# Performance work log

Measured on AMD Instinct MI355X. Metric: run time of the kernel, lower is better.

## Reference

```python
import jax, jax.numpy as jnp
import numpy as np

HIDDEN = 32
ODE_H = 0.1      # rk4 fixed step size (torchdiffeq options step_size=0.1)
ODE_STEPS = 10   # integrate t in [0, 1]


def gcn_conv(x, W, b, edge_index, n):
    """PyG GCNConv: symmetric norm with self-loops; x' = D^-1/2 (A+I) D^-1/2 (x W) + b."""
    h = x @ W                                  # [n, out]
    src, dst = edge_index[0], edge_index[1]
    deg = jnp.ones((n,), h.dtype).at[dst].add(1.0)   # +1 for self-loop
    dinv = jax.lax.rsqrt(deg)
    coef = (dinv[src] * dinv[dst])[:, None]
    agg = jnp.zeros_like(h).at[dst].add(h[src] * coef)
    agg = agg + h * (dinv * dinv)[:, None]     # self-loop term
    return agg + b


def ode_rk4(x0, edge_index, Wg, bg, wt, n):
    """RK4 integration of psi(t,x)=relu(GCN(x)) * sigmoid(t * wt) from t=0 to 1."""
    def f(t, x):
        gate = jax.nn.sigmoid(t * wt)          # [hidden], Linear(1,h,no bias).sigmoid()
        return jax.nn.relu(gcn_conv(x, Wg, bg, edge_index, n)) * gate

    h = ODE_H
    def step(x, t):
        k1 = f(t, x)
        k2 = f(t + h * 0.5, x + (h * 0.5) * k1)
        k3 = f(t + h * 0.5, x + (h * 0.5) * k2)
        k4 = f(t + h, x + h * k3)
        return x + (h / 6.0) * (k1 + 2.0 * k2 + 2.0 * k3 + k4), None

    ts = jnp.arange(ODE_STEPS, dtype=x0.dtype) * h
    xf, _ = jax.lax.scan(step, x0, ts)
    return xf


def setup_inputs() -> dict:
    key = jax.random.key(0)
    ks = jax.random.split(key, 16)
    N, IN, H = 100000, 128, HIDDEN
    E, DE = 1600000, 800000

    inp = {
        "H_t": jax.random.normal(ks[0], (N, IN), jnp.float32),
        "A_pos_t": jax.random.randint(ks[1], (2, E), 0, N),
        "A_neg_t": jax.random.randint(ks[2], (2, E), 0, N),
        "dA_pos": jax.random.randint(ks[3], (2, DE), 0, N),
        "dA_neg": jax.random.randint(ks[4], (2, DE), 0, N),
        # init GCN
        "W_init": jax.random.normal(ks[5], (IN, H), jnp.float32) / np.sqrt(IN),
        "b_init": jnp.zeros((H,), jnp.float32),
        # pos ODE func
        "W_pos": jax.random.normal(ks[6], (H, H), jnp.float32) / np.sqrt(H),
        "b_pos": jnp.zeros((H,), jnp.float32),
        "wt_pos": jax.random.normal(ks[7], (H,), jnp.float32),
        # neg ODE func
        "W_neg": jax.random.normal(ks[8], (H, H), jnp.float32) / np.sqrt(H),
        "b_neg": jnp.zeros((H,), jnp.float32),
        "wt_neg": jax.random.normal(ks[9], (H,), jnp.float32),
        # combine + layernorm
        "W_comb": jax.random.normal(ks[10], (2 * H, H), jnp.float32) / np.sqrt(2 * H),
        "b_comb": jnp.zeros((H,), jnp.float32),
        "ln_g": jnp.ones((H,), jnp.float32),
        "ln_b": jnp.zeros((H,), jnp.float32),
    }
    return inp


def reference(H_t, A_pos_t, A_neg_t, dA_pos, dA_neg,
              W_init, b_init, W_pos, b_pos, wt_pos,
              W_neg, b_neg, wt_neg, W_comb, b_comb, ln_g, ln_b):
    n = H_t.shape[0]
    edges_all = jnp.concatenate([A_pos_t, A_neg_t], axis=1)
    H = jax.nn.relu(gcn_conv(H_t, W_init, b_init, edges_all, n))   # [n, hidden]
    Z_pos = ode_rk4(H, dA_pos, W_pos, b_pos, wt_pos, n)
    Z_neg = ode_rk4(H, dA_neg, W_neg, b_neg, wt_neg, n)
    Z = jnp.concatenate([Z_pos, Z_neg], axis=-1) @ W_comb + b_comb # [n, hidden]
    mu = jnp.mean(Z, axis=-1, keepdims=True)
    var = jnp.var(Z, axis=-1, keepdims=True)
    return (Z - mu) * jax.lax.rsqrt(var + 1e-5) * ln_g + ln_b
```

## Files before the change

### kernel.cpp

```cpp
#include <hip/hip_runtime.h>
#include <math.h>


#define TPB 256
#define SCAN_T 1024
#define IDX_CAP 2048

typedef _Float16 h8 __attribute__((ext_vector_type(8)));
typedef float f8 __attribute__((ext_vector_type(8)));


struct Seg { const int* dst; int n; int* cnt; };
struct FSeg { const int* src; const int* dst; int n; const int* offs; int* cur; };

__global__ void count4(Seg s0, Seg s1, Seg s2, Seg s3) {
    int i = blockIdx.x * blockDim.x + threadIdx.x;
    Seg s; int e;
    if (i < s0.n) { s = s0; e = i; }
    else if (i < s0.n + s1.n) { s = s1; e = i - s0.n; }
    else if (i < s0.n + s1.n + s2.n) { s = s2; e = i - s0.n - s1.n; }
    else if (i < s0.n + s1.n + s2.n + s3.n) { s = s3; e = i - s0.n - s1.n - s2.n; }
    else return;
    atomicAdd(&s.cnt[s.dst[e]], 1);
}

__global__ void fill4(FSeg s0, FSeg s1, FSeg s2, FSeg s3, int* __restrict__ csr) {
    int i = blockIdx.x * blockDim.x + threadIdx.x;
    FSeg s; int e;
    if (i < s0.n) { s = s0; e = i; }
    else if (i < s0.n + s1.n) { s = s1; e = i - s0.n; }
    else if (i < s0.n + s1.n + s2.n) { s = s2; e = i - s0.n - s1.n; }
    else if (i < s0.n + s1.n + s2.n + s3.n) { s = s3; e = i - s0.n - s1.n - s2.n; }
    else return;
    int d = s.dst[e];
    int pos = s.offs[d] + atomicAdd(&s.cur[d], 1);
    csr[pos] = s.src[e];
}

__global__ void dinv_from_cnt(const int* __restrict__ cnt, float* __restrict__ dinv, int n) {
    int i = blockIdx.x * blockDim.x + threadIdx.x;
    if (i < n) dinv[i] = rsqrtf(1.0f + (float)cnt[i]);
}

__global__ void scan_block(const int* __restrict__ in, int n, int* __restrict__ out,
                           int* __restrict__ bsums) {
    __shared__ int sh[SCAN_T];
    int tx = threadIdx.x;
    int g = blockIdx.x * SCAN_T + tx;
    int v = (g < n) ? in[g] : 0;
    sh[tx] = v;
    __syncthreads();
    for (int off = 1; off < SCAN_T; off <<= 1) {
        int t = (tx >= off) ? sh[tx - off] : 0;
        __syncthreads();
        sh[tx] += t;
        __syncthreads();
    }
    if (g < n) out[g] = sh[tx] - v;
    if (tx == SCAN_T - 1) bsums[blockIdx.x] = sh[tx];
}

__global__ void scan_sums(int* __restrict__ bsums, int nb) {
    __shared__ int sh[SCAN_T];
    int tx = threadIdx.x;
    int v = (tx < nb) ? bsums[tx] : 0;
    sh[tx] = v;
    __syncthreads();
    for (int off = 1; off < SCAN_T; off <<= 1) {
        int t = (tx >= off) ? sh[tx - off] : 0;
        __syncthreads();
        sh[tx] += t;
        __syncthreads();
    }
    if (tx < nb) bsums[tx] = sh[tx] - v;
}

__global__ void scan_add(int* __restrict__ offs, const int* __restrict__ bsums, int n, int total) {
    int g = blockIdx.x * blockDim.x + threadIdx.x;
    if (g < n) offs[g] += bsums[g >> 10];
    if (g == 0) offs[n] = total;
}


__global__ void mm32_kernel(const float* __restrict__ x, const float* __restrict__ W,
                            const float* __restrict__ dinv, _Float16* __restrict__ hs, int N) {
    __shared__ float Ws[32][32];
    __shared__ float xs[8][32];
    int tid = threadIdx.x;
    for (int i = tid; i < 32 * 32; i += TPB) Ws[i >> 5][i & 31] = W[i];
    int base = blockIdx.x * 8;
    {
        int idx = base * 32 + tid;
        xs[tid >> 5][tid & 31] = (idx < N * 32) ? x[idx] : 0.0f;
    }
    __syncthreads();
    int row = tid >> 5, c = tid & 31;
    int gr = base + row;
    float acc = 0.0f;
#pragma unroll
    for (int k = 0; k < 32; ++k) acc += xs[row][k] * Ws[k][c];
    if (gr < N) hs[gr * 32 + c] = (_Float16)(acc * dinv[gr]);
}

__global__ void mm128_kernel(const float* __restrict__ x, const float* __restrict__ W,
                             const float* __restrict__ dinv, _Float16* __restrict__ hs, int N) {
    __shared__ float Ws[128][32];
    __shared__ float xs[8][128];
    int tid = threadIdx.x;
    for (int i = tid; i < 128 * 32; i += TPB) Ws[i >> 5][i & 31] = W[i];
    int base = blockIdx.x * 8;
    for (int i = tid; i < 8 * 128; i += TPB) {
        int idx = base * 128 + i;
        xs[i >> 7][i & 127] = (idx < N * 128) ? x[idx] : 0.0f;
    }
    __syncthreads();
    int row = tid >> 5, c = tid & 31;
    int gr = base + row;
    float acc = 0.0f;
#pragma unroll
    for (int k = 0; k < 128; ++k) acc += xs[row][k] * Ws[k][c];
    if (gr < N) hs[gr * 32 + c] = (_Float16)(acc * dinv[gr]);
}


struct Job {
    const int* offs; const int* csr;
    const _Float16* hs_in; _Float16* hs_out;
    const float* dinv; const float* dinv_next;
    const float* bias; const float* wt;
    float* ksum; float* x;
    const float* W;
};

__global__ __launch_bounds__(TPB) void agg_stage(Job jp, Job jn, int nbp, float t,
                                                 int stage, int do_mm, float* __restrict__ x2,
                                                 int N) {
    __shared__ float Ws[32][32];
    __shared__ float xts[64][36];
    __shared__ int sidx[IDX_CAP];
    __shared__ int soffs[65];

    bool isP = blockIdx.x < nbp;
    const Job& J = isP ? jp : jn;
    int bid = isP ? blockIdx.x : (blockIdx.x - nbp);
    int nbase = bid * 64;
    int tid = threadIdx.x;
    int lnode = tid >> 2, q = tid & 3;
    int node = nbase + lnode;
    bool valid = node < N;

    if (do_mm) {
        for (int i = tid; i < 32 * 32; i += TPB) Ws[i >> 5][i & 31] = J.W[i];
    }
    int nend = nbase + 64; if (nend > N) nend = N;
    int e_lo = J.offs[nbase];
    int e_hi = J.offs[nend];
    int cnt = e_hi - e_lo;
    int staged = cnt < IDX_CAP ? cnt : IDX_CAP;
    for (int i = tid; i < staged; i += TPB) sidx[i] = J.csr[e_lo + i];
    if (tid < 65) {
        int ix = nbase + tid; if (ix > N) ix = N;
        soffs[tid] = J.offs[ix];
    }
    __syncthreads();

    f8 xrow;
#pragma unroll
    for (int j = 0; j < 8; ++j) xrow[j] = 0.f;

    if (valid) {
        const h8* hsv = (const h8*)J.hs_in;
        int r0 = soffs[lnode] - e_lo;
        int r1 = soffs[lnode + 1] - e_lo;
        f8 acc = __builtin_convertvector(hsv[node * 4 + q], f8);
        int i = r0;
        int lim = r1 < staged ? r1 : staged;
        for (; i + 4 <= lim; i += 4) {
            h8 v0 = hsv[sidx[i] * 4 + q];
            h8 v1 = hsv[sidx[i + 1] * 4 + q];
            h8 v2 = hsv[sidx[i + 2] * 4 + q];
            h8 v3 = hsv[sidx[i + 3] * 4 + q];
            acc += (__builtin_convertvector(v0, f8) + __builtin_convertvector(v1, f8))
                 + (__builtin_convertvector(v2, f8) + __builtin_convertvector(v3, f8));
        }
        for (; i < lim; ++i)
            acc += __builtin_convertvector(hsv[sidx[i] * 4 + q], f8);
        for (; i < r1; ++i)
            acc += __builtin_convertvector(hsv[J.csr[e_lo + i] * 4 + q], f8);

        float dv = J.dinv[node];
        f8 bb = ((const f8*)J.bias)[q];
        f8 kv;
#pragma unroll
        for (int j = 0; j < 8; ++j) kv[j] = fmaxf(acc[j] * dv + bb[j], 0.f);
        if (J.wt) {
            f8 w = ((const f8*)J.wt)[q];
#pragma unroll
            for (int j = 0; j < 8; ++j) kv[j] *= 1.f / (1.f + expf(-t * w[j]));
        }
        int idx = node * 4 + q;
        f8* x8 = (f8*)J.x;
        f8* ks8 = (f8*)J.ksum;
        if (stage == 0) {
            x8[idx] = kv;
            ((f8*)x2)[idx] = kv;
            xrow = kv;
        } else if (stage == 4) {
            f8 ks = ks8[idx];
            f8 xv = x8[idx];
            const float cc = 0.1f / 6.0f;
#pragma unroll
            for (int j = 0; j < 8; ++j) xv[j] += cc * (ks[j] + kv[j]);
            x8[idx] = xv;
            xrow = xv;
        } else {
            float a = (stage == 3) ? 0.1f : 0.05f;
            f8 xv = x8[idx];
#pragma unroll
            for (int j = 0; j < 8; ++j) xrow[j] = xv[j] + a * kv[j];
            if (stage == 1) {
                ks8[idx] = kv;
            } else {
                f8 ks = ks8[idx];
#pragma unroll
                for (int j = 0; j < 8; ++j) ks[j] += 2.f * kv[j];
                ks8[idx] = ks;
            }
        }
    }

    if (do_mm) {
        if (valid) {
#pragma unroll
            for (int j = 0; j < 8; ++j) xts[lnode][q * 8 + j] = xrow[j];
        }
        __syncthreads();
        if (valid) {
            f8 accm;
#pragma unroll
            for (int j = 0; j < 8; ++j) accm[j] = 0.f;
#pragma unroll
            for (int k = 0; k < 32; ++k) {
                float xv = xts[lnode][k];
                f8 w = *(const f8*)&Ws[k][q * 8];
                accm += xv * w;
            }
            accm *= J.dinv_next[node];
            ((h8*)J.hs_out)[node * 4 + q] = __builtin_convertvector(accm, h8);
        }
    }
}


__global__ void combine_kernel(const float* __restrict__ zp, const float* __restrict__ zn,
                               const float* __restrict__ Wc, const float* __restrict__ bc,
                               const float* __restrict__ g, const float* __restrict__ be,
                               float* __restrict__ out, int N) {
    __shared__ float Ws[64][32];
    __shared__ float zs[8][64];
    int tid = threadIdx.x;
    for (int i = tid; i < 64 * 32; i += TPB) Ws[i >> 5][i & 31] = Wc[i];
    int base = blockIdx.x * 8;
    {
        int r = tid >> 5, c = tid & 31;
        int gr = base + r;
        zs[r][c] = (gr < N) ? zp[gr * 32 + c] : 0.0f;
        zs[r][32 + c] = (gr < N) ? zn[gr * 32 + c] : 0.0f;
    }
    __syncthreads();
    int row = tid >> 5, c = tid & 31;
    int gr = base + row;
    float acc = bc[c];
#pragma unroll
    for (int k = 0; k < 64; ++k) acc += zs[row][k] * Ws[k][c];
    float s = acc, sq = acc * acc;
#pragma unroll
    for (int off = 16; off; off >>= 1) {
        s += __shfl_xor(s, off, 32);
        sq += __shfl_xor(sq, off, 32);
    }
    float mu = s * (1.0f / 32.0f);
    float var = sq * (1.0f / 32.0f) - mu * mu;
    float y = (acc - mu) * rsqrtf(var + 1e-5f) * g[c] + be[c];
    if (gr < N) out[gr * 32 + c] = y;
}


extern "C" void kernel_launch(void* const* d_in, const int* in_sizes, int n_in,
                              void* d_out, int out_size, void* d_ws, size_t ws_size,
                              hipStream_t stream) {
    const float* H_t = (const float*)d_in[0];
    const int* Apos = (const int*)d_in[1];
    const int* Aneg = (const int*)d_in[2];
    const int* dApos = (const int*)d_in[3];
    const int* dAneg = (const int*)d_in[4];
    const float* W_init = (const float*)d_in[5];
    const float* b_init = (const float*)d_in[6];
    const float* W_pos = (const float*)d_in[7];
    const float* b_pos = (const float*)d_in[8];
    const float* wt_pos = (const float*)d_in[9];
    const float* W_neg = (const float*)d_in[10];
    const float* b_neg = (const float*)d_in[11];
    const float* wt_neg = (const float*)d_in[12];
    const float* W_comb = (const float*)d_in[13];
    const float* b_comb = (const float*)d_in[14];
    const float* ln_g = (const float*)d_in[15];
    const float* ln_b = (const float*)d_in[16];

    const int N = in_sizes[0] / 128;
    const int E1 = in_sizes[1] / 2;
    const int E2 = in_sizes[2] / 2;
    const int DE1 = in_sizes[3] / 2;
    const int DE2 = in_sizes[4] / 2;
    const int Etot = E1 + E2 + DE1 + DE2;

    const int* Apos_src = Apos, * Apos_dst = Apos + E1;
    const int* Aneg_src = Aneg, * Aneg_dst = Aneg + E2;
    const int* dApos_src = dApos, * dApos_dst = dApos + DE1;
    const int* dAneg_src = dAneg, * dAneg_dst = dAneg + DE2;

    const size_t n32 = (size_t)N * 32;
    const size_t szf = n32 * 4;
    const size_t szh = n32 * 2;
    auto al = [](size_t b) { return (b + 255) & ~(size_t)255; };

    size_t small_bytes = 3 * al((size_t)(3 * N) * 4)
                       + al((3 * (size_t)N + 1) * 4)
                       + al((size_t)Etot * 4)
                       + al(SCAN_T * 4);
    size_t need_merged = 4 * al(szf) + 4 * al(szh) + small_bytes;
    bool merged = ws_size >= need_merged + 4096;

    char* p = (char*)d_ws;
    auto alloc = [&](size_t bytes) -> void* {
        void* r = (void*)p;
        p += al(bytes);
        return r;
    };
    float* x_pos = (float*)alloc(szf);
    float* x_neg = (float*)alloc(szf);
    float* ksum_p = (float*)alloc(szf);
    float* ksum_n = merged ? (float*)alloc(szf) : ksum_p;
    _Float16* hs_pa = (_Float16*)alloc(szh);
    _Float16* hs_pb = (_Float16*)alloc(szh);
    _Float16* hs_na = merged ? (_Float16*)alloc(szh) : hs_pa;
    _Float16* hs_nb = merged ? (_Float16*)alloc(szh) : hs_pb;
    float* dinv3 = (float*)alloc((size_t)(3 * N) * 4);
    int* cnt3 = (int*)alloc((size_t)(3 * N) * 4);
    int* cur3 = (int*)alloc((size_t)(3 * N) * 4);
    int* offs3 = (int*)alloc((3 * (size_t)N + 1) * 4);
    int* csr3 = (int*)alloc((size_t)Etot * 4);
    int* bsums = (int*)alloc(SCAN_T * 4);

    size_t used = (size_t)(p - (char*)d_ws);
    if (used > ws_size) used = ws_size;

    hipMemsetAsync(d_ws, 0, used, stream);

    float* dinv_all = dinv3, * dinv_pos = dinv3 + N, * dinv_neg = dinv3 + 2 * N;
    int* cnt_all = cnt3, * cnt_pos = cnt3 + N, * cnt_neg = cnt3 + 2 * N;
    int* cur_all = cur3, * cur_pos = cur3 + N, * cur_neg = cur3 + 2 * N;
    const int* offs_all = offs3, * offs_pos = offs3 + N, * offs_neg = offs3 + 2 * N;

    dim3 blk(TPB);
    auto gblk = [](int n) { return dim3((n + TPB - 1) / TPB); };
    dim3 grid_rows((N + 7) / 8);
    const int nb64 = (N + 63) / 64;
    const int n3 = 3 * N;
    const int nbs = (n3 + SCAN_T - 1) / SCAN_T;

    {
        Seg s0 = { Apos_dst, E1, cnt_all };
        Seg s1 = { Aneg_dst, E2, cnt_all };
        Seg s2 = { dApos_dst, DE1, cnt_pos };
        Seg s3 = { dAneg_dst, DE2, cnt_neg };
        count4<<<gblk(Etot), blk, 0, stream>>>(s0, s1, s2, s3);
    }
    dinv_from_cnt<<<gblk(n3), blk, 0, stream>>>(cnt3, dinv3, n3);
    scan_block<<<nbs, SCAN_T, 0, stream>>>(cnt3, n3, offs3, bsums);
    scan_sums<<<1, SCAN_T, 0, stream>>>(bsums, nbs);
    scan_add<<<gblk(n3), blk, 0, stream>>>(offs3, bsums, n3, Etot);
    {
        FSeg f0 = { Apos_src, Apos_dst, E1, offs_all, cur_all };
        FSeg f1 = { Aneg_src, Aneg_dst, E2, offs_all, cur_all };
        FSeg f2 = { dApos_src, dApos_dst, DE1, offs_pos, cur_pos };
        FSeg f3 = { dAneg_src, dAneg_dst, DE2, offs_neg, cur_neg };
        fill4<<<gblk(Etot), blk, 0, stream>>>(f0, f1, f2, f3, csr3);
    }

    auto mkjob = [&](const int* offs, const _Float16* hs_in, _Float16* hs_out,
                     const float* dinv, const float* dinv_next, const float* bias,
                     const float* wt, float* ksum, float* x, const float* W) {
        Job j; j.offs = offs; j.csr = csr3; j.hs_in = hs_in; j.hs_out = hs_out;
        j.dinv = dinv; j.dinv_next = dinv_next; j.bias = bias; j.wt = wt;
        j.ksum = ksum; j.x = x; j.W = W; return j;
    };

    mm128_kernel<<<grid_rows, blk, 0, stream>>>(H_t, W_init, dinv_all, hs_pa, N);
    {
        Job j0 = mkjob(offs_all, hs_pa, hs_pb, dinv_all, dinv_pos, b_init,
                       nullptr, nullptr, x_pos, W_pos);
        agg_stage<<<nb64, blk, 0, stream>>>(j0, j0, nb64, 0.0f, 0, 1, x_neg, N);
    }

    if (merged) {
        mm32_kernel<<<grid_rows, blk, 0, stream>>>(x_neg, W_neg, dinv_neg, hs_nb, N);
        for (int s = 0; s < 10; ++s) {
            float t0 = 0.1f * (float)s;
            int last_mm = (s == 9) ? 0 : 1;
            Job p1 = mkjob(offs_pos, hs_pb, hs_pa, dinv_pos, dinv_pos, b_pos, wt_pos, ksum_p, x_pos, W_pos);
            Job n1 = mkjob(offs_neg, hs_nb, hs_na, dinv_neg, dinv_neg, b_neg, wt_neg, ksum_n, x_neg, W_neg);
            agg_stage<<<2 * nb64, blk, 0, stream>>>(p1, n1, nb64, t0, 1, 1, nullptr, N);
            Job p2 = p1; p2.hs_in = hs_pa; p2.hs_out = hs_pb;
            Job n2 = n1; n2.hs_in = hs_na; n2.hs_out = hs_nb;
            agg_stage<<<2 * nb64, blk, 0, stream>>>(p2, n2, nb64, t0 + 0.05f, 2, 1, nullptr, N);
            agg_stage<<<2 * nb64, blk, 0, stream>>>(p1, n1, nb64, t0 + 0.05f, 3, 1, nullptr, N);
            agg_stage<<<2 * nb64, blk, 0, stream>>>(p2, n2, nb64, t0 + 0.1f, 4, last_mm, nullptr, N);
        }
    } else {
        for (int ode = 0; ode < 2; ++ode) {
            float* x = ode ? x_neg : x_pos;
            const float* W = ode ? W_neg : W_pos;
            const float* b = ode ? b_neg : b_pos;
            const float* wt = ode ? wt_neg : wt_pos;
            const float* dinv = ode ? dinv_neg : dinv_pos;
            const int* offs = ode ? offs_neg : offs_pos;
            if (ode == 1) {
                mm32_kernel<<<grid_rows, blk, 0, stream>>>(x, W, dinv, hs_pb, N);
            }
            for (int s = 0; s < 10; ++s) {
                float t0 = 0.1f * (float)s;
                int last_mm = (s == 9) ? 0 : 1;
                Job j1 = mkjob(offs, hs_pb, hs_pa, dinv, dinv, b, wt, ksum_p, x, W);
                Job j2 = j1; j2.hs_in = hs_pa; j2.hs_out = hs_pb;
                agg_stage<<<nb64, blk, 0, stream>>>(j1, j1, nb64, t0, 1, 1, nullptr, N);
                agg_stage<<<nb64, blk, 0, stream>>>(j2, j2, nb64, t0 + 0.05f, 2, 1, nullptr, N);
                agg_stage<<<nb64, blk, 0, stream>>>(j1, j1, nb64, t0 + 0.05f, 3, 1, nullptr, N);
                agg_stage<<<nb64, blk, 0, stream>>>(j2, j2, nb64, t0 + 0.1f, 4, last_mm, nullptr, N);
            }
        }
    }

    combine_kernel<<<grid_rows, blk, 0, stream>>>(x_pos, x_neg, W_comb, b_comb, ln_g, ln_b,
                                                  (float*)d_out, N);
}
```

Measured before the change: 2.185 ms.

## Build CSR via two-pass radix bucketing and drop LDS index staging in aggregation

```diff
diff --git a/kernel.cpp b/kernel.cpp
--- a/kernel.cpp
+++ b/kernel.cpp
@@ -4,24 +4,25 @@
 
 #define TPB 256
 #define SCAN_T 1024
-#define IDX_CAP 2048
+#define RB 512
+#define PA_TILE 4096
 
 typedef _Float16 h8 __attribute__((ext_vector_type(8)));
 typedef float f8 __attribute__((ext_vector_type(8)));
 
 
-struct Seg { const int* dst; int n; int* cnt; };
+struct SegG { const int* src; const int* dst; int n; int goff; };
 struct FSeg { const int* src; const int* dst; int n; const int* offs; int* cur; };
 
-__global__ void count4(Seg s0, Seg s1, Seg s2, Seg s3) {
+__global__ void count4(SegG s0, SegG s1, SegG s2, SegG s3, int* __restrict__ cnt3) {
     int i = blockIdx.x * blockDim.x + threadIdx.x;
-    Seg s; int e;
+    SegG s; int e;
     if (i < s0.n) { s = s0; e = i; }
     else if (i < s0.n + s1.n) { s = s1; e = i - s0.n; }
     else if (i < s0.n + s1.n + s2.n) { s = s2; e = i - s0.n - s1.n; }
     else if (i < s0.n + s1.n + s2.n + s3.n) { s = s3; e = i - s0.n - s1.n - s2.n; }
     else return;
-    atomicAdd(&s.cnt[s.dst[e]], 1);
+    atomicAdd(&cnt3[s.goff + s.dst[e]], 1);
 }
 
 __global__ void fill4(FSeg s0, FSeg s1, FSeg s2, FSeg s3, int* __restrict__ csr) {
@@ -81,6 +82,83 @@
     if (g == 0) offs[n] = total;
 }
 
+__global__ void init_stage_cur(const int* __restrict__ offs3, int* __restrict__ stage_cur,
+                               int B, int n3) {
+    int b = blockIdx.x * blockDim.x + threadIdx.x;
+    if (b < B) {
+        int k = b << 10; if (k > n3) k = n3;
+        stage_cur[b] = offs3[k];
+    }
+}
+
+__global__ __launch_bounds__(TPB) void passA(SegG s0, SegG s1, SegG s2, SegG s3,
+                                             int* __restrict__ stage_cur,
+                                             int* __restrict__ staging, int Etot) {
+    __shared__ int lh[RB];
+    __shared__ int lbase[RB];
+    int tid = threadIdx.x;
+    int base = blockIdx.x * PA_TILE;
+    int t1 = s0.n, t2 = t1 + s1.n, t3 = t2 + s2.n;
+
+    for (int b = tid; b < RB; b += TPB) lh[b] = 0;
+    __syncthreads();
+
+    int gds[16], srcs[16];
+#pragma unroll
+    for (int k = 0; k < 16; ++k) {
+        int i = base + k * TPB + tid;
+        gds[k] = -1;
+        if (i < Etot) {
+            SegG s; int e;
+            if (i < t1) { s = s0; e = i; }
+            else if (i < t2) { s = s1; e = i - t1; }
+            else if (i < t3) { s = s2; e = i - t2; }
+            else { s = s3; e = i - t3; }
+            int gd = s.goff + s.dst[e];
+            gds[k] = gd;
+            srcs[k] = s.src[e];
+            atomicAdd(&lh[gd >> 10], 1);
+        }
+    }
+    __syncthreads();
+    for (int b = tid; b < RB; b += TPB) {
+        int c = lh[b];
+        lbase[b] = c ? atomicAdd(&stage_cur[b], c) : 0;
+    }
+    __syncthreads();
+    for (int b = tid; b < RB; b += TPB) lh[b] = 0;
+    __syncthreads();
+#pragma unroll
+    for (int k = 0; k < 16; ++k) {
+        int gd = gds[k];
+        if (gd >= 0) {
+            int b = gd >> 10;
+            int r = atomicAdd(&lh[b], 1);
+            staging[lbase[b] + r] = ((gd & 1023) << 17) | srcs[k];
+        }
+    }
+}
+
+__global__ __launch_bounds__(TPB) void passB(const int* __restrict__ staging,
+                                             const int* __restrict__ offs3,
+                                             int* __restrict__ cur3,
+                                             int* __restrict__ csr3, int n3) {
+    int b = blockIdx.x >> 3, sl = blockIdx.x & 7;
+    int k0 = b << 10;
+    int k1 = k0 + 1024; if (k1 > n3) k1 = n3;
+    if (k0 >= n3) return;
+    int lo = offs3[k0], hi = offs3[k1];
+    int len = hi - lo;
+    int c0 = lo + (int)((long long)len * sl / 8);
+    int c1 = lo + (int)((long long)len * (sl + 1) / 8);
+    for (int i = c0 + threadIdx.x; i < c1; i += TPB) {
+        int ent = staging[i];
+        int gd = k0 + (ent >> 17);
+        int pos = offs3[gd] + atomicAdd(&cur3[gd], 1);
+        csr3[pos] = ent & 0x1FFFF;
+    }
+}
+
 
 __global__ void mm32_kernel(const float* __restrict__ x, const float* __restrict__ W,
                             const float* __restrict__ dinv, _Float16* __restrict__ hs, int N) {
@@ -137,7 +215,6 @@
                                                  int N) {
     __shared__ float Ws[32][32];
     __shared__ float xts[64][36];
-    __shared__ int sidx[IDX_CAP];
     __shared__ int soffs[65];
 
     bool isP = blockIdx.x < nbp;
@@ -152,12 +229,6 @@
     if (do_mm) {
         for (int i = tid; i < 32 * 32; i += TPB) Ws[i >> 5][i & 31] = J.W[i];
     }
-    int nend = nbase + 64; if (nend > N) nend = N;
-    int e_lo = J.offs[nbase];
-    int e_hi = J.offs[nend];
-    int cnt = e_hi - e_lo;
-    int staged = cnt < IDX_CAP ? cnt : IDX_CAP;
-    for (int i = tid; i < staged; i += TPB) sidx[i] = J.csr[e_lo + i];
     if (tid < 65) {
         int ix = nbase + tid; if (ix > N) ix = N;
         soffs[tid] = J.offs[ix];
@@ -170,23 +241,21 @@
 
     if (valid) {
         const h8* hsv = (const h8*)J.hs_in;
-        int r0 = soffs[lnode] - e_lo;
-        int r1 = soffs[lnode + 1] - e_lo;
+        const int* __restrict__ csr = J.csr;
+        int r0 = soffs[lnode], r1 = soffs[lnode + 1];
         f8 acc = __builtin_convertvector(hsv[node * 4 + q], f8);
         int i = r0;
-        int lim = r1 < staged ? r1 : staged;
-        for (; i + 4 <= lim; i += 4) {
-            h8 v0 = hsv[sidx[i] * 4 + q];
-            h8 v1 = hsv[sidx[i + 1] * 4 + q];
-            h8 v2 = hsv[sidx[i + 2] * 4 + q];
-            h8 v3 = hsv[sidx[i + 3] * 4 + q];
+        for (; i + 4 <= r1; i += 4) {
+            int s0 = csr[i], s1 = csr[i + 1], s2 = csr[i + 2], s3 = csr[i + 3];
+            h8 v0 = hsv[s0 * 4 + q];
+            h8 v1 = hsv[s1 * 4 + q];
+            h8 v2 = hsv[s2 * 4 + q];
+            h8 v3 = hsv[s3 * 4 + q];
             acc += (__builtin_convertvector(v0, f8) + __builtin_convertvector(v1, f8))
                  + (__builtin_convertvector(v2, f8) + __builtin_convertvector(v3, f8));
         }
-        for (; i < lim; ++i)
-            acc += __builtin_convertvector(hsv[sidx[i] * 4 + q], f8);
         for (; i < r1; ++i)
-            acc += __builtin_convertvector(hsv[J.csr[e_lo + i] * 4 + q], f8);
+            acc += __builtin_convertvector(hsv[csr[i] * 4 + q], f8);
 
         float dv = J.dinv[node];
         f8 bb = ((const f8*)J.bias)[q];
@@ -329,7 +398,10 @@
                        + al((size_t)Etot * 4)
                        + al(SCAN_T * 4);
     size_t need_merged = 4 * al(szf) + 4 * al(szh) + small_bytes;
+    size_t need_radix = need_merged + al((size_t)Etot * 4) + al(RB * 4);
     bool merged = ws_size >= need_merged + 4096;
+    bool radix = merged && (ws_size >= need_radix + 4096) && (N <= 131071)
+                 && (((3 * N + 1023) >> 10) <= RB);
 
     char* p = (char*)d_ws;
     auto alloc = [&](size_t bytes) -> void* {
@@ -351,6 +423,8 @@
     int* offs3 = (int*)alloc((3 * (size_t)N + 1) * 4);
     int* csr3 = (int*)alloc((size_t)Etot * 4);
     int* bsums = (int*)alloc(SCAN_T * 4);
+    int* staging = radix ? (int*)alloc((size_t)Etot * 4) : nullptr;
+    int* stage_cur = radix ? (int*)alloc(RB * 4) : nullptr;
 
     size_t used = (size_t)(p - (char*)d_ws);
     if (used > ws_size) used = ws_size;
@@ -358,8 +432,6 @@
     hipMemsetAsync(d_ws, 0, used, stream);
 
     float* dinv_all = dinv3, * dinv_pos = dinv3 + N, * dinv_neg = dinv3 + 2 * N;
-    int* cnt_all = cnt3, * cnt_pos = cnt3 + N, * cnt_neg = cnt3 + 2 * N;
-    int* cur_all = cur3, * cur_pos = cur3 + N, * cur_neg = cur3 + 2 * N;
     const int* offs_all = offs3, * offs_pos = offs3 + N, * offs_neg = offs3 + 2 * N;
 
     dim3 blk(TPB);
@@ -368,23 +440,27 @@
     const int nb64 = (N + 63) / 64;
     const int n3 = 3 * N;
     const int nbs = (n3 + SCAN_T - 1) / SCAN_T;
-
-    {
-        Seg s0 = { Apos_dst, E1, cnt_all };
-        Seg s1 = { Aneg_dst, E2, cnt_all };
-        Seg s2 = { dApos_dst, DE1, cnt_pos };
-        Seg s3 = { dAneg_dst, DE2, cnt_neg };
-        count4<<<gblk(Etot), blk, 0, stream>>>(s0, s1, s2, s3);
-    }
+    const int B = (n3 + 1023) >> 10;
+
+    SegG s0 = { Apos_src, Apos_dst, E1, 0 };
+    SegG s1 = { Aneg_src, Aneg_dst, E2, 0 };
+    SegG s2 = { dApos_src, dApos_dst, DE1, N };
+    SegG s3 = { dAneg_src, dAneg_dst, DE2, 2 * N };
+    count4<<<gblk(Etot), blk, 0, stream>>>(s0, s1, s2, s3, cnt3);
     dinv_from_cnt<<<gblk(n3), blk, 0, stream>>>(cnt3, dinv3, n3);
     scan_block<<<nbs, SCAN_T, 0, stream>>>(cnt3, n3, offs3, bsums);
     scan_sums<<<1, SCAN_T, 0, stream>>>(bsums, nbs);
     scan_add<<<gblk(n3), blk, 0, stream>>>(offs3, bsums, n3, Etot);
-    {
-        FSeg f0 = { Apos_src, Apos_dst, E1, offs_all, cur_all };
-        FSeg f1 = { Aneg_src, Aneg_dst, E2, offs_all, cur_all };
-        FSeg f2 = { dApos_src, dApos_dst, DE1, offs_pos, cur_pos };
-        FSeg f3 = { dAneg_src, dAneg_dst, DE2, offs_neg, cur_neg };
+    if (radix) {
+        init_stage_cur<<<gblk(B), blk, 0, stream>>>(offs3, stage_cur, B, n3);
+        passA<<<(Etot + PA_TILE - 1) / PA_TILE, blk, 0, stream>>>(s0, s1, s2, s3,
+                                                                  stage_cur, staging, Etot);
+        passB<<<B * 8, blk, 0, stream>>>(staging, offs3, cur3, csr3, n3);
+    } else {
+        FSeg f0 = { Apos_src, Apos_dst, E1, offs3, cur3 };
+        FSeg f1 = { Aneg_src, Aneg_dst, E2, offs3, cur3 };
+        FSeg f2 = { dApos_src, dApos_dst, DE1, offs3 + N, cur3 + N };
+        FSeg f3 = { dAneg_src, dAneg_dst, DE2, offs3 + 2 * N, cur3 + 2 * N };
         fill4<<<gblk(Etot), blk, 0, stream>>>(f0, f1, f2, f3, csr3);
     }
 
```

Result: slower. 2.325 ms (+6.4%).

## Store RK4 ksum in fp16, drop LDS index staging, XCD-split pos/neg blocks

Applied to the files above, without the earlier changes.

```diff
diff --git a/kernel.cpp b/kernel.cpp
--- a/kernel.cpp
+++ b/kernel.cpp
@@ -4,24 +4,23 @@
 
 #define TPB 256
 #define SCAN_T 1024
-#define IDX_CAP 2048
 
 typedef _Float16 h8 __attribute__((ext_vector_type(8)));
 typedef float f8 __attribute__((ext_vector_type(8)));
 
 
-struct Seg { const int* dst; int n; int* cnt; };
+struct SegG { const int* src; const int* dst; int n; int goff; };
 struct FSeg { const int* src; const int* dst; int n; const int* offs; int* cur; };
 
-__global__ void count4(Seg s0, Seg s1, Seg s2, Seg s3) {
+__global__ void count4(SegG s0, SegG s1, SegG s2, SegG s3, int* __restrict__ cnt3) {
     int i = blockIdx.x * blockDim.x + threadIdx.x;
-    Seg s; int e;
+    SegG s; int e;
     if (i < s0.n) { s = s0; e = i; }
     else if (i < s0.n + s1.n) { s = s1; e = i - s0.n; }
     else if (i < s0.n + s1.n + s2.n) { s = s2; e = i - s0.n - s1.n; }
     else if (i < s0.n + s1.n + s2.n + s3.n) { s = s3; e = i - s0.n - s1.n - s2.n; }
     else return;
-    atomicAdd(&s.cnt[s.dst[e]], 1);
+    atomicAdd(&cnt3[s.goff + s.dst[e]], 1);
 }
 
 __global__ void fill4(FSeg s0, FSeg s1, FSeg s2, FSeg s3, int* __restrict__ csr) {
@@ -128,21 +127,28 @@
     const _Float16* hs_in; _Float16* hs_out;
     const float* dinv; const float* dinv_next;
     const float* bias; const float* wt;
-    float* ksum; float* x;
+    _Float16* ksum; float* x;
     const float* W;
 };
 
-__global__ __launch_bounds__(TPB) void agg_stage(Job jp, Job jn, int nbp, float t,
-                                                 int stage, int do_mm, float* __restrict__ x2,
-                                                 int N) {
+__global__ __launch_bounds__(TPB) void agg_stage(Job jp, Job jn, int nbg, float t,
+                                                 int stage, int do_mm, int split,
+                                                 float* __restrict__ x2, int N) {
     __shared__ float Ws[32][32];
     __shared__ float xts[64][36];
-    __shared__ int sidx[IDX_CAP];
     __shared__ int soffs[65];
 
-    bool isP = blockIdx.x < nbp;
+    bool isP; int bid;
+    if (split) {
+        int xcd = blockIdx.x & 7;
+        isP = xcd < 4;
+        bid = ((int)blockIdx.x >> 3) * 4 + (xcd & 3);
+        if (bid >= nbg) return;
+    } else {
+        isP = (int)blockIdx.x < nbg;
+        bid = isP ? blockIdx.x : (blockIdx.x - nbg);
+    }
     const Job& J = isP ? jp : jn;
-    int bid = isP ? blockIdx.x : (blockIdx.x - nbp);
     int nbase = bid * 64;
     int tid = threadIdx.x;
     int lnode = tid >> 2, q = tid & 3;
@@ -152,12 +158,6 @@
     if (do_mm) {
         for (int i = tid; i < 32 * 32; i += TPB) Ws[i >> 5][i & 31] = J.W[i];
     }
-    int nend = nbase + 64; if (nend > N) nend = N;
-    int e_lo = J.offs[nbase];
-    int e_hi = J.offs[nend];
-    int cnt = e_hi - e_lo;
-    int staged = cnt < IDX_CAP ? cnt : IDX_CAP;
-    for (int i = tid; i < staged; i += TPB) sidx[i] = J.csr[e_lo + i];
     if (tid < 65) {
         int ix = nbase + tid; if (ix > N) ix = N;
         soffs[tid] = J.offs[ix];
@@ -170,23 +170,21 @@
 
     if (valid) {
         const h8* hsv = (const h8*)J.hs_in;
-        int r0 = soffs[lnode] - e_lo;
-        int r1 = soffs[lnode + 1] - e_lo;
+        const int* __restrict__ csr = J.csr;
+        int r0 = soffs[lnode], r1 = soffs[lnode + 1];
         f8 acc = __builtin_convertvector(hsv[node * 4 + q], f8);
         int i = r0;
-        int lim = r1 < staged ? r1 : staged;
-        for (; i + 4 <= lim; i += 4) {
-            h8 v0 = hsv[sidx[i] * 4 + q];
-            h8 v1 = hsv[sidx[i + 1] * 4 + q];
-            h8 v2 = hsv[sidx[i + 2] * 4 + q];
-            h8 v3 = hsv[sidx[i + 3] * 4 + q];
+        for (; i + 4 <= r1; i += 4) {
+            int s0 = csr[i], s1 = csr[i + 1], s2 = csr[i + 2], s3 = csr[i + 3];
+            h8 v0 = hsv[s0 * 4 + q];
+            h8 v1 = hsv[s1 * 4 + q];
+            h8 v2 = hsv[s2 * 4 + q];
+            h8 v3 = hsv[s3 * 4 + q];
             acc += (__builtin_convertvector(v0, f8) + __builtin_convertvector(v1, f8))
                  + (__builtin_convertvector(v2, f8) + __builtin_convertvector(v3, f8));
         }
-        for (; i < lim; ++i)
-            acc += __builtin_convertvector(hsv[sidx[i] * 4 + q], f8);
         for (; i < r1; ++i)
-            acc += __builtin_convertvector(hsv[J.csr[e_lo + i] * 4 + q], f8);
+            acc += __builtin_convertvector(hsv[csr[i] * 4 + q], f8);
 
         float dv = J.dinv[node];
         f8 bb = ((const f8*)J.bias)[q];
@@ -200,13 +198,13 @@
         }
         int idx = node * 4 + q;
         f8* x8 = (f8*)J.x;
-        f8* ks8 = (f8*)J.ksum;
+        h8* ks8 = (h8*)J.ksum;
         if (stage == 0) {
             x8[idx] = kv;
             ((f8*)x2)[idx] = kv;
             xrow = kv;
         } else if (stage == 4) {
-            f8 ks = ks8[idx];
+            f8 ks = __builtin_convertvector(ks8[idx], f8);
             f8 xv = x8[idx];
             const float cc = 0.1f / 6.0f;
 #pragma unroll
@@ -219,12 +217,12 @@
 #pragma unroll
             for (int j = 0; j < 8; ++j) xrow[j] = xv[j] + a * kv[j];
             if (stage == 1) {
-                ks8[idx] = kv;
+                ks8[idx] = __builtin_convertvector(kv, h8);
             } else {
-                f8 ks = ks8[idx];
+                f8 ks = __builtin_convertvector(ks8[idx], f8);
 #pragma unroll
                 for (int j = 0; j < 8; ++j) ks[j] += 2.f * kv[j];
-                ks8[idx] = ks;
+                ks8[idx] = __builtin_convertvector(ks, h8);
             }
         }
     }
@@ -328,7 +326,7 @@
                        + al((3 * (size_t)N + 1) * 4)
                        + al((size_t)Etot * 4)
                        + al(SCAN_T * 4);
-    size_t need_merged = 4 * al(szf) + 4 * al(szh) + small_bytes;
+    size_t need_merged = 2 * al(szf) + 6 * al(szh) + small_bytes;
     bool merged = ws_size >= need_merged + 4096;
 
     char* p = (char*)d_ws;
@@ -339,8 +337,8 @@
     };
     float* x_pos = (float*)alloc(szf);
     float* x_neg = (float*)alloc(szf);
-    float* ksum_p = (float*)alloc(szf);
-    float* ksum_n = merged ? (float*)alloc(szf) : ksum_p;
+    _Float16* ksum_p = (_Float16*)alloc(szh);
+    _Float16* ksum_n = merged ? (_Float16*)alloc(szh) : ksum_p;
     _Float16* hs_pa = (_Float16*)alloc(szh);
     _Float16* hs_pb = (_Float16*)alloc(szh);
     _Float16* hs_na = merged ? (_Float16*)alloc(szh) : hs_pa;
@@ -358,8 +356,6 @@
     hipMemsetAsync(d_ws, 0, used, stream);
 
     float* dinv_all = dinv3, * dinv_pos = dinv3 + N, * dinv_neg = dinv3 + 2 * N;
-    int* cnt_all = cnt3, * cnt_pos = cnt3 + N, * cnt_neg = cnt3 + 2 * N;
-    int* cur_all = cur3, * cur_pos = cur3 + N, * cur_neg = cur3 + 2 * N;
     const int* offs_all = offs3, * offs_pos = offs3 + N, * offs_neg = offs3 + 2 * N;
 
     dim3 blk(TPB);
@@ -368,29 +364,28 @@
     const int nb64 = (N + 63) / 64;
     const int n3 = 3 * N;
     const int nbs = (n3 + SCAN_T - 1) / SCAN_T;
-
-    {
-        Seg s0 = { Apos_dst, E1, cnt_all };
-        Seg s1 = { Aneg_dst, E2, cnt_all };
-        Seg s2 = { dApos_dst, DE1, cnt_pos };
-        Seg s3 = { dAneg_dst, DE2, cnt_neg };
-        count4<<<gblk(Etot), blk, 0, stream>>>(s0, s1, s2, s3);
-    }
+    const int nsplit = ((nb64 + 3) / 4) * 8;
+
+    SegG s0 = { Apos_src, Apos_dst, E1, 0 };
+    SegG s1 = { Aneg_src, Aneg_dst, E2, 0 };
+    SegG s2 = { dApos_src, dApos_dst, DE1, N };
+    SegG s3 = { dAneg_src, dAneg_dst, DE2, 2 * N };
+    count4<<<gblk(Etot), blk, 0, stream>>>(s0, s1, s2, s3, cnt3);
     dinv_from_cnt<<<gblk(n3), blk, 0, stream>>>(cnt3, dinv3, n3);
     scan_block<<<nbs, SCAN_T, 0, stream>>>(cnt3, n3, offs3, bsums);
     scan_sums<<<1, SCAN_T, 0, stream>>>(bsums, nbs);
     scan_add<<<gblk(n3), blk, 0, stream>>>(offs3, bsums, n3, Etot);
     {
-        FSeg f0 = { Apos_src, Apos_dst, E1, offs_all, cur_all };
-        FSeg f1 = { Aneg_src, Aneg_dst, E2, offs_all, cur_all };
-        FSeg f2 = { dApos_src, dApos_dst, DE1, offs_pos, cur_pos };
-        FSeg f3 = { dAneg_src, dAneg_dst, DE2, offs_neg, cur_neg };
+        FSeg f0 = { Apos_src, Apos_dst, E1, offs3, cur3 };
+        FSeg f1 = { Aneg_src, Aneg_dst, E2, offs3, cur3 };
+        FSeg f2 = { dApos_src, dApos_dst, DE1, offs3 + N, cur3 + N };
+        FSeg f3 = { dAneg_src, dAneg_dst, DE2, offs3 + 2 * N, cur3 + 2 * N };
         fill4<<<gblk(Etot), blk, 0, stream>>>(f0, f1, f2, f3, csr3);
     }
 
     auto mkjob = [&](const int* offs, const _Float16* hs_in, _Float16* hs_out,
                      const float* dinv, const float* dinv_next, const float* bias,
-                     const float* wt, float* ksum, float* x, const float* W) {
+                     const float* wt, _Float16* ksum, float* x, const float* W) {
         Job j; j.offs = offs; j.csr = csr3; j.hs_in = hs_in; j.hs_out = hs_out;
         j.dinv = dinv; j.dinv_next = dinv_next; j.bias = bias; j.wt = wt;
         j.ksum = ksum; j.x = x; j.W = W; return j;
@@ -400,7 +395,7 @@
     {
         Job j0 = mkjob(offs_all, hs_pa, hs_pb, dinv_all, dinv_pos, b_init,
                        nullptr, nullptr, x_pos, W_pos);
-        agg_stage<<<nb64, blk, 0, stream>>>(j0, j0, nb64, 0.0f, 0, 1, x_neg, N);
+        agg_stage<<<nb64, blk, 0, stream>>>(j0, j0, nb64, 0.0f, 0, 1, 0, x_neg, N);
     }
 
     if (merged) {
@@ -410,12 +405,12 @@
             int last_mm = (s == 9) ? 0 : 1;
             Job p1 = mkjob(offs_pos, hs_pb, hs_pa, dinv_pos, dinv_pos, b_pos, wt_pos, ksum_p, x_pos, W_pos);
             Job n1 = mkjob(offs_neg, hs_nb, hs_na, dinv_neg, dinv_neg, b_neg, wt_neg, ksum_n, x_neg, W_neg);
-            agg_stage<<<2 * nb64, blk, 0, stream>>>(p1, n1, nb64, t0, 1, 1, nullptr, N);
+            agg_stage<<<nsplit, blk, 0, stream>>>(p1, n1, nb64, t0, 1, 1, 1, nullptr, N);
             Job p2 = p1; p2.hs_in = hs_pa; p2.hs_out = hs_pb;
             Job n2 = n1; n2.hs_in = hs_na; n2.hs_out = hs_nb;
-            agg_stage<<<2 * nb64, blk, 0, stream>>>(p2, n2, nb64, t0 + 0.05f, 2, 1, nullptr, N);
-            agg_stage<<<2 * nb64, blk, 0, stream>>>(p1, n1, nb64, t0 + 0.05f, 3, 1, nullptr, N);
-            agg_stage<<<2 * nb64, blk, 0, stream>>>(p2, n2, nb64, t0 + 0.1f, 4, last_mm, nullptr, N);
+            agg_stage<<<nsplit, blk, 0, stream>>>(p2, n2, nb64, t0 + 0.05f, 2, 1, 1, nullptr, N);
+            agg_stage<<<nsplit, blk, 0, stream>>>(p1, n1, nb64, t0 + 0.05f, 3, 1, 1, nullptr, N);
+            agg_stage<<<nsplit, blk, 0, stream>>>(p2, n2, nb64, t0 + 0.1f, 4, last_mm, 1, nullptr, N);
         }
     } else {
         for (int ode = 0; ode < 2; ++ode) {
@@ -433,10 +428,10 @@
                 int last_mm = (s == 9) ? 0 : 1;
                 Job j1 = mkjob(offs, hs_pb, hs_pa, dinv, dinv, b, wt, ksum_p, x, W);
                 Job j2 = j1; j2.hs_in = hs_pa; j2.hs_out = hs_pb;
-                agg_stage<<<nb64, blk, 0, stream>>>(j1, j1, nb64, t0, 1, 1, nullptr, N);
-                agg_stage<<<nb64, blk, 0, stream>>>(j2, j2, nb64, t0 + 0.05f, 2, 1, nullptr, N);
-                agg_stage<<<nb64, blk, 0, stream>>>(j1, j1, nb64, t0 + 0.05f, 3, 1, nullptr, N);
-                agg_stage<<<nb64, blk, 0, stream>>>(j2, j2, nb64, t0 + 0.1f, 4, last_mm, nullptr, N);
+                agg_stage<<<nb64, blk, 0, stream>>>(j1, j1, nb64, t0, 1, 1, 0, nullptr, N);
+                agg_stage<<<nb64, blk, 0, stream>>>(j2, j2, nb64, t0 + 0.05f, 2, 1, 0, nullptr, N);
+                agg_stage<<<nb64, blk, 0, stream>>>(j1, j1, nb64, t0 + 0.05f, 3, 1, 0, nullptr, N);
+                agg_stage<<<nb64, blk, 0, stream>>>(j2, j2, nb64, t0 + 0.1f, 4, last_mm, 0, nullptr, N);
             }
         }
     }
```

Measured after the change: 2.144 ms. About the same (-1.9%).
